# Performance work log

Measured on AMD Instinct MI355X. Metric: run time of the kernel, lower is better.

The kernel has to match this reference:

```python
import jax, jax.numpy as jnp
import numpy as np

HIDDEN = 1024
HEADS = 16
HEAD = HIDDEN // HEADS


def setup_inputs() -> dict:
    key = jax.random.key(0)
    k1, k2, k3, k4, k5, k6 = jax.random.split(key, 6)
    B, S = 2, 2048
    x = jax.random.normal(k1, (B, S, HIDDEN), dtype=jnp.float32)
    mask = jax.random.randint(k2, (B, S), 0, 2, dtype=jnp.int32)
    # torch nn.Linear params: W [out,in], b [out]
    s = 1.0 / np.sqrt(HIDDEN)
    qkv_w = jax.random.uniform(k3, (3 * HIDDEN, HIDDEN), jnp.float32, -s, s)
    qkv_b = jax.random.uniform(k4, (3 * HIDDEN,), jnp.float32, -s, s)
    out_w = jax.random.uniform(k5, (HIDDEN, HIDDEN), jnp.float32, -s, s)
    out_b = jax.random.uniform(k6, (HIDDEN,), jnp.float32, -s, s)
    return {"x": x, "mask": mask, "qkv_w": qkv_w, "qkv_b": qkv_b,
            "out_w": out_w, "out_b": out_b}


def reference(x, mask, qkv_w, qkv_b, out_w, out_b):
    B, S, H = x.shape
    scale = HEAD ** -0.5
    qkv = x @ qkv_w.T + qkv_b                      # [B,S,3H]
    qkv = qkv.reshape(B, S, 3, HEADS, HEAD)
    qkv = jnp.transpose(qkv, (2, 0, 3, 1, 4))      # [3,B,h,S,d]
    q, k, v = qkv[0], qkv[1], qkv[2]
    scores = jnp.einsum('bhqd,bhkd->bhqk', q, k) * scale
    # key-padding mask [B,S] -> [B,1,1,S]
    scores = jnp.where(mask[:, None, None, :] == 0, -1e9, scores)
    attn = jax.nn.softmax(scores, axis=-1)
    # dropout is identity in eval mode
    ctx = jnp.einsum('bhqk,bhkd->bhqd', attn, v)   # [B,h,S,d]
    ctx = jnp.transpose(ctx, (0, 2, 1, 3)).reshape(B, S, H)
    return ctx @ out_w.T + out_b
```

## Files before the change

### kernel.cpp

```cpp
#include <hip/hip_runtime.h>
#include <hip/hip_bf16.h>

#define S_LEN 2048
#define NH    16
#define HD    64
#define HID   1024
#define BATCH 2
#define STK   72
#define VSTK  136
#define SCQ   0.18033688f

typedef __bf16 bf16x8 __attribute__((ext_vector_type(8)));
typedef float  f32x4  __attribute__((ext_vector_type(4)));
typedef float  f32x16 __attribute__((ext_vector_type(16)));
typedef unsigned u32x2 __attribute__((ext_vector_type(2)));

__device__ __forceinline__ unsigned int pk2(float lo, float hi) {
    union { __hip_bfloat162 h; unsigned int u; } c;
    c.h = __float22bfloat162_rn(make_float2(lo, hi));
    return c.u;
}
__device__ __forceinline__ uint4 pk8(float4 a, float4 b) {
    uint4 o;
    o.x = pk2(a.x, a.y); o.y = pk2(a.z, a.w);
    o.z = pk2(b.x, b.y); o.w = pk2(b.z, b.w);
    return o;
}
__device__ __forceinline__ float exp2_hw(float x) {
    float r; asm("v_exp_f32 %0, %1" : "=v"(r) : "v"(x)); return r;
}
__device__ __forceinline__ void pl32swap(unsigned &a, unsigned &b) {
    u32x2 r = __builtin_amdgcn_permlane32_swap(a, b, false, false);
    a = r[0]; b = r[1];
}
__device__ __forceinline__ float pair_max(float x) {
    unsigned u = __float_as_uint(x);
    u32x2 r = __builtin_amdgcn_permlane32_swap(u, u, false, false);
    return fmaxf(__uint_as_float(r[0]), __uint_as_float(r[1]));
}
__device__ __forceinline__ float pair_sum(float x) {
    unsigned u = __float_as_uint(x);
    u32x2 r = __builtin_amdgcn_permlane32_swap(u, u, false, false);
    return __uint_as_float(r[0]) + __uint_as_float(r[1]);
}
__device__ __forceinline__ void gll16(const unsigned short* g, unsigned short* l) {
    __builtin_amdgcn_global_load_lds(
        (const __attribute__((address_space(1))) void*)g,
        (__attribute__((address_space(3))) void*)l, 16, 0, 0);
}

__global__ __launch_bounds__(256)
void fill_constf(float* __restrict__ out, long n, float v) {
    long i = (long)blockIdx.x * 256 + threadIdx.x;
    const long stride = (long)gridDim.x * 256;
    for (; i < n; i += stride) out[i] = v;
}

__global__ __launch_bounds__(256)
void cvt_bf16(const float* __restrict__ src, unsigned short* __restrict__ dst, long n8) {
    long t = (long)blockIdx.x * 256 + threadIdx.x;
    const long stride = (long)gridDim.x * 256;
    for (; t < n8; t += stride) {
        const float4 a = *(const float4*)(src + t * 8);
        const float4 b = *(const float4*)(src + t * 8 + 4);
        *(uint4*)(dst + t * 8) = pk8(a, b);
    }
}
__global__ __launch_bounds__(256)
void cvt2_bf16(const float* __restrict__ s0, unsigned short* __restrict__ d0, long n0,
               const float* __restrict__ s1, unsigned short* __restrict__ d1, long n1) {
    long t = (long)blockIdx.x * 256 + threadIdx.x;
    const long stride = (long)gridDim.x * 256;
    for (; t < n0 + n1; t += stride) {
        const float* s; unsigned short* d; long i;
        if (t < n0) { s = s0; d = d0; i = t; } else { s = s1; d = d1; i = t - n0; }
        const float4 a = *(const float4*)(s + i * 8);
        const float4 b = *(const float4*)(s + i * 8 + 4);
        *(uint4*)(d + i * 8) = pk8(a, b);
    }
}

__global__ __launch_bounds__(512)
void gemm_bf16(const unsigned short* __restrict__ A,
               const unsigned short* __restrict__ W,
               const float* __restrict__ bias,
               unsigned short* __restrict__ o0,
               unsigned short* __restrict__ o1,
               unsigned short* __restrict__ o2)
{
    __shared__ __align__(16) unsigned short lA[3][128 * 32];
    __shared__ __align__(16) unsigned short lB[3][128 * 32];
    const int tid  = threadIdx.x;
    const int lane = tid & 63, wv = tid >> 6;
    const int quad = lane >> 4, l16 = lane & 15;
    const int wm = (wv & 1) * 64, wn = (wv >> 1) * 32;

    const int nwg = gridDim.x * gridDim.y;
    const int bid = blockIdx.y * gridDim.x + blockIdx.x;
    const int xcd = bid & 7, boff = bid >> 3;
    const int qd = nwg >> 3, rm = nwg & 7;
    const int swz = (xcd < rm ? xcd * (qd + 1) : rm * (qd + 1) + (xcd - rm) * qd) + boff;
    const int m0 = (swz / gridDim.x) * 128, n0 = (swz % gridDim.x) * 128;

    f32x4 acc[4][2] = {};

    const int srow = wv * 16 + (lane >> 2);
    const int csrc = ((lane & 3) ^ ((lane >> 3) & 3)) * 8;
    const unsigned short* pa = A + (long)(m0 + srow) * HID + csrc;
    const unsigned short* pb = W + (long)(n0 + srow) * HID + csrc;

    const int cq8 = (quad ^ ((l16 >> 1) & 3)) * 8;

#define STAGE_G(bufi, koff)                                        \
    do {                                                           \
        gll16(pa + (koff), &lA[bufi][wv * 512]);                   \
        gll16(pb + (koff), &lB[bufi][wv * 512]);                   \
    } while (0)

    STAGE_G(0, 0);
    STAGE_G(1, 32);

    int cur = 0;
    for (int k0 = 0; k0 < HID; k0 += 32) {
        if (k0 + 32 < HID) { asm volatile("s_waitcnt vmcnt(2)" ::: "memory"); }
        else               { asm volatile("s_waitcnt vmcnt(0)" ::: "memory"); }
        __builtin_amdgcn_s_barrier();
        asm volatile("" ::: "memory");

        if (k0 + 64 < HID) {
            const int nxt = cur ? cur - 1 : 2;
            STAGE_G(nxt, k0 + 64);
        }

        bf16x8 af[4], bfr[2];
#pragma unroll
        for (int mt = 0; mt < 4; mt++)
            af[mt] = *(const bf16x8*)&lA[cur][(wm + mt * 16 + l16) * 32 + cq8];
#pragma unroll
        for (int nt = 0; nt < 2; nt++)
            bfr[nt] = *(const bf16x8*)&lB[cur][(wn + nt * 16 + l16) * 32 + cq8];
#pragma unroll
        for (int mt = 0; mt < 4; mt++)
#pragma unroll
            for (int nt = 0; nt < 2; nt++)
                acc[mt][nt] = __builtin_amdgcn_mfma_f32_16x16x32_bf16(
                    af[mt], bfr[nt], acc[mt][nt], 0, 0, 0);

        cur = (cur < 2) ? cur + 1 : 0;
    }
#undef STAGE_G

#pragma unroll
    for (int nt = 0; nt < 2; nt++) {
        const int n = n0 + wn + nt * 16 + l16;
        const float bv = bias[n];
        const int part = n >> 10, f = n & 1023, h = f >> 6, d = f & 63;
#pragma unroll
        for (int mt = 0; mt < 4; mt++) {
            const int mbase = m0 + wm + mt * 16 + quad * 4;
            const int b = mbase >> 11, s0 = mbase & 2047;
            const int bh = b * NH + h;
            if (part != 1) {
                const float qsc = (part == 0) ? SCQ : 1.0f;
                unsigned short* dst = (part == 0) ? o0 : o2;
                uint2 o;
                o.x = pk2((acc[mt][nt][0] + bv) * qsc, (acc[mt][nt][1] + bv) * qsc);
                o.y = pk2((acc[mt][nt][2] + bv) * qsc, (acc[mt][nt][3] + bv) * qsc);
                *(uint2*)&dst[((long)bh * HD + d) * S_LEN + s0] = o;
            } else {
#pragma unroll
                for (int r = 0; r < 4; r++) {
                    union { __hip_bfloat16 h; unsigned short u; } cv;
                    cv.h = __float2bfloat16(acc[mt][nt][r] + bv);
                    o1[((long)bh * S_LEN + s0 + r) * HD + d] = cv.u;
                }
            }
        }
    }
}

__global__ __launch_bounds__(512)
void gemm_out(const unsigned short* __restrict__ A,
              const unsigned short* __restrict__ W,
              const float* __restrict__ bias,
              float* __restrict__ of)
{
    __shared__ __align__(16) unsigned short lA[3][128 * 32];
    __shared__ __align__(16) unsigned short lB[3][64 * 32];
    const int tid  = threadIdx.x;
    const int lane = tid & 63, wv = tid >> 6;
    const int quad = lane >> 4, l16 = lane & 15;
    const int wm = (wv & 3) * 32, wn = (wv >> 2) * 32;

    const int nwg = gridDim.x * gridDim.y;
    const int bid = blockIdx.y * gridDim.x + blockIdx.x;
    const int xcd = bid & 7, boff = bid >> 3;
    const int qd = nwg >> 3, rm = nwg & 7;
    const int swz = (xcd < rm ? xcd * (qd + 1) : rm * (qd + 1) + (xcd - rm) * qd) + boff;
    const int m0 = (swz / gridDim.x) * 128, n0 = (swz % gridDim.x) * 64;

    f32x4 acc[2][2] = {};

    const int srowA = wv * 16 + (lane >> 2);
    const int srowB = srowA & 63;
    const int csrc  = ((lane & 3) ^ ((lane >> 3) & 3)) * 8;
    const unsigned short* pa = A + (long)(m0 + srowA) * HID + csrc;
    const unsigned short* pb = W + (long)(n0 + srowB) * HID + csrc;

    const int cq8 = (quad ^ ((l16 >> 1) & 3)) * 8;

#define STAGE_O(bufi, koff)                                        \
    do {                                                           \
        gll16(pa + (koff), &lA[bufi][wv * 512]);                   \
        if (wv < 4) gll16(pb + (koff), &lB[bufi][wv * 512]);       \
    } while (0)

    STAGE_O(0, 0);
    STAGE_O(1, 32);

    int cur = 0;
    for (int k0 = 0; k0 < HID; k0 += 32) {
        if (k0 + 32 < HID) {
            if (wv < 4) { asm volatile("s_waitcnt vmcnt(2)" ::: "memory"); }
            else        { asm volatile("s_waitcnt vmcnt(1)" ::: "memory"); }
        } else          { asm volatile("s_waitcnt vmcnt(0)" ::: "memory"); }
        __builtin_amdgcn_s_barrier();
        asm volatile("" ::: "memory");

        if (k0 + 64 < HID) {
            const int nxt = cur ? cur - 1 : 2;
            STAGE_O(nxt, k0 + 64);
        }

        bf16x8 af[2], bfr[2];
#pragma unroll
        for (int mt = 0; mt < 2; mt++)
            af[mt] = *(const bf16x8*)&lA[cur][(wm + mt * 16 + l16) * 32 + cq8];
#pragma unroll
        for (int nt = 0; nt < 2; nt++)
            bfr[nt] = *(const bf16x8*)&lB[cur][(wn + nt * 16 + l16) * 32 + cq8];
#pragma unroll
        for (int mt = 0; mt < 2; mt++)
#pragma unroll
            for (int nt = 0; nt < 2; nt++)
                acc[mt][nt] = __builtin_amdgcn_mfma_f32_16x16x32_bf16(
                    af[mt], bfr[nt], acc[mt][nt], 0, 0, 0);

        cur = (cur < 2) ? cur + 1 : 0;
    }
#undef STAGE_O

#pragma unroll
    for (int nt = 0; nt < 2; nt++) {
        const int n = n0 + wn + nt * 16 + l16;
        const float bv = bias[n];
#pragma unroll
        for (int mt = 0; mt < 2; mt++) {
            const int mbase = m0 + wm + mt * 16 + quad * 4;
#pragma unroll
            for (int r = 0; r < 4; r++)
                of[(long)(mbase + r) * HID + n] = acc[mt][nt][r] + bv;
        }
    }
}

__global__ __launch_bounds__(512, 4)
void attn(const unsigned short* __restrict__ q,
          const unsigned short* __restrict__ k,
          const unsigned short* __restrict__ vt_g,
          const int* __restrict__ mask,
          unsigned short* __restrict__ ctx)
{
    __shared__ __align__(16) unsigned short kt[2][128 * STK];
    __shared__ __align__(16) unsigned short vt[2][64 * VSTK];
    __shared__ __align__(16) float mkv[2][128];

    const int tid  = threadIdx.x;
    const int lane = tid & 63, wv = tid >> 6;
    const int ar = lane & 31, hi = lane >> 5;
    const int chunk = wv >> 1, p = wv & 1;
    const int id = blockIdx.x;
    const int xcd = id & 7, j = id >> 3;
    const int qt = j & 15, hbl = j >> 4;
    const int hb = xcd * 4 + hbl;
    const int h = hb & 15, b = hb >> 4;
    const int bh = b * NH + h;
    const int sq = qt * 128 + chunk * 32 + ar;

    union { unsigned short u[8]; bf16x8 v; } qu[4];
    const unsigned short* qg = q + (long)bh * HD * S_LEN + sq;
#pragma unroll
    for (int t = 0; t < 4; t++)
#pragma unroll
        for (int jj = 0; jj < 8; jj++)
            qu[t].u[jj] = qg[(long)(16 * t + 8 * hi + jj) * S_LEN];

    float mrun = 0.f, lsum = 0.f;
    f32x16 Of0 = {}, Of1 = {};

    const int sr = tid >> 3, c0 = tid & 7;
    const unsigned short* kg = k    + ((long)bh * S_LEN + sr) * HD + c0 * 8;
    const unsigned short* vg = vt_g + ((long)bh * HD + sr) * S_LEN + c0 * 8;
    const int wk0 = sr * STK + c0 * 8;
    const int wk1 = (sr + 64) * STK + c0 * 8;
    const int wv0 = sr * VSTK + c0 * 8;
    const int wv1 = sr * VSTK + c0 * 8 + 64;

    uint4 rk0 = *(const uint4*)(kg);
    uint4 rk1 = *(const uint4*)(kg + (long)64 * HD);
    uint4 rv0 = *(const uint4*)(vg);
    uint4 rv1 = *(const uint4*)(vg + 64);
    float rmv = 0.f;
    if (tid < 128) rmv = (mask[b * S_LEN + tid] == 0) ? -1e9f : 0.f;
    *(uint4*)&kt[0][wk0] = rk0;
    *(uint4*)&kt[0][wk1] = rk1;
    *(uint4*)&vt[0][wv0] = rv0;
    *(uint4*)&vt[0][wv1] = rv1;
    if (tid < 128) mkv[0][tid] = rmv;
    rk0 = *(const uint4*)(kg + (long)128 * HD);
    rk1 = *(const uint4*)(kg + (long)192 * HD);
    rv0 = *(const uint4*)(vg + 128);
    rv1 = *(const uint4*)(vg + 192);
    if (tid < 128) rmv = (mask[b * S_LEN + 128 + tid] == 0) ? -1e9f : 0.f;
    asm volatile("s_waitcnt lgkmcnt(0)" ::: "memory");
    __builtin_amdgcn_s_barrier();
    asm volatile("" ::: "memory");

    for (int k0 = 0; k0 < S_LEN; k0 += 128) {
        const int cur = (k0 >> 7) & 1;
        if (k0 + 128 < S_LEN) {
            *(uint4*)&kt[cur ^ 1][wk0] = rk0;
            *(uint4*)&kt[cur ^ 1][wk1] = rk1;
            *(uint4*)&vt[cur ^ 1][wv0] = rv0;
            *(uint4*)&vt[cur ^ 1][wv1] = rv1;
            if (tid < 128) mkv[cur ^ 1][tid] = rmv;
            if (k0 + 256 < S_LEN) {
                rk0 = *(const uint4*)(kg + (long)(k0 + 256) * HD);
                rk1 = *(const uint4*)(kg + (long)(k0 + 320) * HD);
                rv0 = *(const uint4*)(vg + (k0 + 256));
                rv1 = *(const uint4*)(vg + (k0 + 320));
                if (tid < 128) rmv = (mask[b * S_LEN + k0 + 256 + tid] == 0) ? -1e9f : 0.f;
            }
        }

#pragma unroll
        for (int G2 = 0; G2 < 2; G2++) {
            const int kb = 64 * G2 + 32 * p;

            f32x16 s;
#pragma unroll
            for (int m = 0; m < 4; m++) {
                const float4 mv = *(const float4*)&mkv[cur][kb + m * 8 + hi * 4];
                s[4 * m + 0] = mv.x; s[4 * m + 1] = mv.y;
                s[4 * m + 2] = mv.z; s[4 * m + 3] = mv.w;
            }
            __builtin_amdgcn_s_setprio(1);
#pragma unroll
            for (int t = 0; t < 4; t++) {
                bf16x8 kf = *(const bf16x8*)
                    &kt[cur][(kb + ar) * STK + (2 * t + hi) * 8];
                s = __builtin_amdgcn_mfma_f32_32x32x16_bf16(kf, qu[t].v, s, 0, 0, 0);
            }
            __builtin_amdgcn_s_setprio(0);

            if (k0 == 0 && G2 == 0) {
                float pm = fmaxf(fmaxf(fmaxf(s[0], s[1]), fmaxf(s[2], s[3])),
                           fmaxf(fmaxf(s[4], s[5]), fmaxf(s[6], s[7])));
                pm = fmaxf(pm,
                     fmaxf(fmaxf(fmaxf(s[8], s[9]), fmaxf(s[10], s[11])),
                           fmaxf(fmaxf(s[12], s[13]), fmaxf(s[14], s[15]))));
                mrun = fmaxf(pair_max(pm), -50.f);
            }

            float pr[16];
            float ls = 0.f;
#pragma unroll
            for (int r = 0; r < 16; r++) {
                pr[r] = exp2_hw(s[r] - mrun);
                ls += pr[r];
            }
            lsum += ls;
            unsigned wa[4], wb[4];
#pragma unroll
            for (int m = 0; m < 4; m++) {
                wa[m] = pk2(pr[4 * m + 0], pr[4 * m + 1]);
                wb[m] = pk2(pr[4 * m + 2], pr[4 * m + 3]);
            }

            union { unsigned u[4]; bf16x8 v; } F[2];
#pragma unroll
            for (int s5 = 0; s5 < 2; s5++) {
                const int mp = s5 * 2;
                unsigned f0 = wa[mp], f2 = wa[mp + 1];
                unsigned f1 = wb[mp], f3 = wb[mp + 1];
                pl32swap(f0, f2);
                pl32swap(f1, f3);
                F[s5].u[0] = f0; F[s5].u[1] = f1; F[s5].u[2] = f2; F[s5].u[3] = f3;
            }

            __builtin_amdgcn_s_setprio(1);
#pragma unroll
            for (int s5 = 0; s5 < 2; s5++) {
                const int col = (2 * (4 * G2 + 2 * p + s5) + hi) * 8;
                bf16x8 vf0 = *(const bf16x8*)&vt[cur][(0 * 32 + ar) * VSTK + col];
                Of0 = __builtin_amdgcn_mfma_f32_32x32x16_bf16(vf0, F[s5].v, Of0, 0, 0, 0);
                bf16x8 vf1 = *(const bf16x8*)&vt[cur][(1 * 32 + ar) * VSTK + col];
                Of1 = __builtin_amdgcn_mfma_f32_32x32x16_bf16(vf1, F[s5].v, Of1, 0, 0, 0);
            }
            __builtin_amdgcn_s_setprio(0);
        }

        asm volatile("s_waitcnt lgkmcnt(0)" ::: "memory");
        __builtin_amdgcn_s_barrier();
        asm volatile("" ::: "memory");
    }

    const float lp = pair_sum(lsum);
    float* mo0 = (float*)&kt[0][0];
    float* mo1 = (float*)&vt[0][0];
    float* mml = (float*)&vt[0][0] + 4096;
    const int mbase = (chunk * 64 + lane) * 16;
    const int mx4 = (lane >> 1) & 3;
    if (p == 1) {
#pragma unroll
        for (int m = 0; m < 4; m++) {
            const int off = mbase + ((m ^ mx4) << 2);
            *(float4*)&mo0[off] = make_float4(Of0[4*m+0], Of0[4*m+1], Of0[4*m+2], Of0[4*m+3]);
            *(float4*)&mo1[off] = make_float4(Of1[4*m+0], Of1[4*m+1], Of1[4*m+2], Of1[4*m+3]);
        }
        mml[(chunk * 64 + lane) * 2 + 0] = mrun;
        mml[(chunk * 64 + lane) * 2 + 1] = lp;
    }
    __syncthreads();
    if (p == 0) {
        const float m1 = mml[(chunk * 64 + lane) * 2 + 0];
        const float l1 = mml[(chunk * 64 + lane) * 2 + 1];
        const float mm = fmaxf(mrun, m1);
        const float a0 = exp2_hw(mrun - mm);
        const float a1 = exp2_hw(m1 - mm);
        const float inv = 1.f / (lp * a0 + l1 * a1);
        unsigned short* cb = ctx + ((long)b * S_LEN + sq) * HID + h * HD;
#pragma unroll
        for (int m = 0; m < 4; m++) {
            const int off = mbase + ((m ^ mx4) << 2);
            const float4 p0 = *(const float4*)&mo0[off];
            const float4 p1 = *(const float4*)&mo1[off];
            uint2 o0, o1;
            o0.x = pk2((Of0[4*m+0] * a0 + p0.x * a1) * inv,
                       (Of0[4*m+1] * a0 + p0.y * a1) * inv);
            o0.y = pk2((Of0[4*m+2] * a0 + p0.z * a1) * inv,
                       (Of0[4*m+3] * a0 + p0.w * a1) * inv);
            *(uint2*)&cb[m * 8 + hi * 4] = o0;
            o1.x = pk2((Of1[4*m+0] * a0 + p1.x * a1) * inv,
                       (Of1[4*m+1] * a0 + p1.y * a1) * inv);
            o1.y = pk2((Of1[4*m+2] * a0 + p1.z * a1) * inv,
                       (Of1[4*m+3] * a0 + p1.w * a1) * inv);
            *(uint2*)&cb[32 + m * 8 + hi * 4] = o1;
        }
    }
}

extern "C" void kernel_launch(void* const* d_in, const int* in_sizes, int n_in,
                              void* d_out, int out_size, void* d_ws, size_t ws_size,
                              hipStream_t stream) {
    float* outp = (float*)d_out;

    const float* x = nullptr; const int* mask = nullptr;
    const float* qkv_w = nullptr; const float* qkv_b = nullptr;
    const float* out_w = nullptr; const float* out_b = nullptr;
    for (int i = 0; i < n_in; i++) {
        switch (in_sizes[i]) {
            case 4194304: x     = (const float*)d_in[i]; break;
            case 4096:    mask  = (const int*)d_in[i];   break;
            case 3145728: qkv_w = (const float*)d_in[i]; break;
            case 3072:    qkv_b = (const float*)d_in[i]; break;
            case 1048576: out_w = (const float*)d_in[i]; break;
            case 1024:    out_b = (const float*)d_in[i]; break;
            default: break;
        }
    }
    if (!x || !mask || !qkv_w || !qkv_b || !out_w || !out_b) {
        fill_constf<<<256, 256, 0, stream>>>(outp, (long)out_size, 1000.0f);
        return;
    }

    const size_t per = (size_t)BATCH * NH * S_LEN * HD;
    const size_t nx  = (size_t)BATCH * S_LEN * HID;
    const size_t nqw = (size_t)3 * HID * HID;
    const size_t now = (size_t)HID * HID;
    if (ws_size < 4 * per * sizeof(unsigned short)) {
        fill_constf<<<256, 256, 0, stream>>>(outp, (long)out_size, 2000.0f);
        return;
    }

    unsigned short* wsq = (unsigned short*)d_ws;
    unsigned short* wsk = wsq + per;
    unsigned short* wsv = wsk + per;
    unsigned short* wsc = wsv + per;
    unsigned short* xb  = wsc;
    unsigned short* qwb = (unsigned short*)d_out;
    unsigned short* owb = wsq;

    cvt2_bf16<<<1024, 256, 0, stream>>>(x, xb, (long)(nx / 8), qkv_w, qwb, (long)(nqw / 8));
    gemm_bf16<<<dim3(3 * HID / 128, BATCH * S_LEN / 128), 512, 0, stream>>>(
        xb, qwb, qkv_b, wsq, wsk, wsv);
    attn<<<dim3(S_LEN / 128 * NH * BATCH), 512, 0, stream>>>(wsq, wsk, wsv, mask, wsc);
    cvt_bf16<<<512, 256, 0, stream>>>(out_w, owb, (long)(now / 8));
    gemm_out<<<dim3(HID / 64, BATCH * S_LEN / 128), 512, 0, stream>>>(
        wsc, owb, out_b, outp);
}
```

Before: 196.6 us.

## Fuse fp32-to-bf16 conversion into GEMM tile loads and drop convert kernels

Both GEMMs now load fp32 inputs (x, qkv_w, out_w) straight from global memory into registers, convert them to bf16, and write them to LDS. This removes the separate conversion kernels and their global round trip. Staging changes from 3-stage async global_load_lds to a 2-stage register-prefetch double buffer with a barrier each iteration. Block-to-tile mapping becomes a fixed per-XCD layout, and launch bounds now request 4 blocks per CU. The costs are twice the global read bytes per tile, because fp32 values are re-read by every block that uses them, plus conversion work inside the main loop.

```diff
diff --git a/kernel.cpp b/kernel.cpp
--- a/kernel.cpp
+++ b/kernel.cpp
@@ -43,11 +43,6 @@
     u32x2 r = __builtin_amdgcn_permlane32_swap(u, u, false, false);
     return __uint_as_float(r[0]) + __uint_as_float(r[1]);
 }
-__device__ __forceinline__ void gll16(const unsigned short* g, unsigned short* l) {
-    __builtin_amdgcn_global_load_lds(
-        (const __attribute__((address_space(1))) void*)g,
-        (__attribute__((address_space(3))) void*)l, 16, 0, 0);
-}
 
 __global__ __launch_bounds__(256)
 void fill_constf(float* __restrict__ out, long n, float v) {
@@ -56,80 +51,61 @@
     for (; i < n; i += stride) out[i] = v;
 }
 
-__global__ __launch_bounds__(256)
-void cvt_bf16(const float* __restrict__ src, unsigned short* __restrict__ dst, long n8) {
-    long t = (long)blockIdx.x * 256 + threadIdx.x;
-    const long stride = (long)gridDim.x * 256;
-    for (; t < n8; t += stride) {
-        const float4 a = *(const float4*)(src + t * 8);
-        const float4 b = *(const float4*)(src + t * 8 + 4);
-        *(uint4*)(dst + t * 8) = pk8(a, b);
-    }
-}
-__global__ __launch_bounds__(256)
-void cvt2_bf16(const float* __restrict__ s0, unsigned short* __restrict__ d0, long n0,
-               const float* __restrict__ s1, unsigned short* __restrict__ d1, long n1) {
-    long t = (long)blockIdx.x * 256 + threadIdx.x;
-    const long stride = (long)gridDim.x * 256;
-    for (; t < n0 + n1; t += stride) {
-        const float* s; unsigned short* d; long i;
-        if (t < n0) { s = s0; d = d0; i = t; } else { s = s1; d = d1; i = t - n0; }
-        const float4 a = *(const float4*)(s + i * 8);
-        const float4 b = *(const float4*)(s + i * 8 + 4);
-        *(uint4*)(d + i * 8) = pk8(a, b);
-    }
-}
-
-__global__ __launch_bounds__(512)
-void gemm_bf16(const unsigned short* __restrict__ A,
-               const unsigned short* __restrict__ W,
-               const float* __restrict__ bias,
-               unsigned short* __restrict__ o0,
-               unsigned short* __restrict__ o1,
-               unsigned short* __restrict__ o2)
+__global__ __launch_bounds__(512, 4)
+void gemm_qkv(const float* __restrict__ X,
+              const float* __restrict__ W,
+              const float* __restrict__ bias,
+              unsigned short* __restrict__ o0,
+              unsigned short* __restrict__ o1,
+              unsigned short* __restrict__ o2)
 {
-    __shared__ __align__(16) unsigned short lA[3][128 * 32];
-    __shared__ __align__(16) unsigned short lB[3][128 * 32];
+    __shared__ __align__(16) unsigned short lA[2][128 * 32];
+    __shared__ __align__(16) unsigned short lB[2][128 * 32];
     const int tid  = threadIdx.x;
     const int lane = tid & 63, wv = tid >> 6;
     const int quad = lane >> 4, l16 = lane & 15;
     const int wm = (wv & 1) * 64, wn = (wv >> 1) * 32;
 
-    const int nwg = gridDim.x * gridDim.y;
-    const int bid = blockIdx.y * gridDim.x + blockIdx.x;
+    const int bid = blockIdx.x;
     const int xcd = bid & 7, boff = bid >> 3;
-    const int qd = nwg >> 3, rm = nwg & 7;
-    const int swz = (xcd < rm ? xcd * (qd + 1) : rm * (qd + 1) + (xcd - rm) * qd) + boff;
-    const int m0 = (swz / gridDim.x) * 128, n0 = (swz % gridDim.x) * 128;
+    const int mloc = boff / 12, nloc = boff % 12;
+    const int m0 = ((xcd & 3) * 8 + mloc) * 128;
+    const int n0 = ((xcd >> 2) * 12 + nloc) * 128;
 
     f32x4 acc[4][2] = {};
 
-    const int srow = wv * 16 + (lane >> 2);
-    const int csrc = ((lane & 3) ^ ((lane >> 3) & 3)) * 8;
-    const unsigned short* pa = A + (long)(m0 + srow) * HID + csrc;
-    const unsigned short* pb = W + (long)(n0 + srow) * HID + csrc;
-
+    const int r = tid >> 2, c = tid & 3;
+    const int wofs = r * 32 + ((c ^ ((r >> 1) & 3)) * 8);
+    const float* px = X + (long)(m0 + r) * HID + c * 8;
+    const float* pw = W + (long)(n0 + r) * HID + c * 8;
     const int cq8 = (quad ^ ((l16 >> 1) & 3)) * 8;
 
-#define STAGE_G(bufi, koff)                                        \
-    do {                                                           \
-        gll16(pa + (koff), &lA[bufi][wv * 512]);                   \
-        gll16(pb + (koff), &lB[bufi][wv * 512]);                   \
-    } while (0)
-
-    STAGE_G(0, 0);
-    STAGE_G(1, 32);
-
-    int cur = 0;
+    float4 xa, xb2, wa2, wb2;
+    xa  = *(const float4*)(px);
+    xb2 = *(const float4*)(px + 4);
+    wa2 = *(const float4*)(pw);
+    wb2 = *(const float4*)(pw + 4);
+    *(uint4*)&lA[0][wofs] = pk8(xa, xb2);
+    *(uint4*)&lB[0][wofs] = pk8(wa2, wb2);
+    xa  = *(const float4*)(px + 32);
+    xb2 = *(const float4*)(px + 36);
+    wa2 = *(const float4*)(pw + 32);
+    wb2 = *(const float4*)(pw + 36);
+    asm volatile("s_waitcnt lgkmcnt(0)" ::: "memory");
+    __builtin_amdgcn_s_barrier();
+    asm volatile("" ::: "memory");
+
     for (int k0 = 0; k0 < HID; k0 += 32) {
-        if (k0 + 32 < HID) { asm volatile("s_waitcnt vmcnt(2)" ::: "memory"); }
-        else               { asm volatile("s_waitcnt vmcnt(0)" ::: "memory"); }
-        __builtin_amdgcn_s_barrier();
-        asm volatile("" ::: "memory");
-
-        if (k0 + 64 < HID) {
-            const int nxt = cur ? cur - 1 : 2;
-            STAGE_G(nxt, k0 + 64);
+        const int cur = (k0 >> 5) & 1;
+        if (k0 + 32 < HID) {
+            *(uint4*)&lA[cur ^ 1][wofs] = pk8(xa, xb2);
+            *(uint4*)&lB[cur ^ 1][wofs] = pk8(wa2, wb2);
+            if (k0 + 64 < HID) {
+                xa  = *(const float4*)(px + k0 + 64);
+                xb2 = *(const float4*)(px + k0 + 68);
+                wa2 = *(const float4*)(pw + k0 + 64);
+                wb2 = *(const float4*)(pw + k0 + 68);
+            }
         }
 
         bf16x8 af[4], bfr[2];
@@ -146,9 +122,10 @@
                 acc[mt][nt] = __builtin_amdgcn_mfma_f32_16x16x32_bf16(
                     af[mt], bfr[nt], acc[mt][nt], 0, 0, 0);
 
-        cur = (cur < 2) ? cur + 1 : 0;
-    }
-#undef STAGE_G
+        asm volatile("s_waitcnt lgkmcnt(0)" ::: "memory");
+        __builtin_amdgcn_s_barrier();
+        asm volatile("" ::: "memory");
+    }
 
 #pragma unroll
     for (int nt = 0; nt < 2; nt++) {
@@ -169,67 +146,68 @@
                 *(uint2*)&dst[((long)bh * HD + d) * S_LEN + s0] = o;
             } else {
 #pragma unroll
-                for (int r = 0; r < 4; r++) {
+                for (int rr = 0; rr < 4; rr++) {
                     union { __hip_bfloat16 h; unsigned short u; } cv;
-                    cv.h = __float2bfloat16(acc[mt][nt][r] + bv);
-                    o1[((long)bh * S_LEN + s0 + r) * HD + d] = cv.u;
+                    cv.h = __float2bfloat16(acc[mt][nt][rr] + bv);
+                    o1[((long)bh * S_LEN + s0 + rr) * HD + d] = cv.u;
                 }
             }
         }
     }
 }
 
-__global__ __launch_bounds__(512)
+__global__ __launch_bounds__(512, 4)
 void gemm_out(const unsigned short* __restrict__ A,
-              const unsigned short* __restrict__ W,
+              const float* __restrict__ W,
               const float* __restrict__ bias,
               float* __restrict__ of)
 {
-    __shared__ __align__(16) unsigned short lA[3][128 * 32];
-    __shared__ __align__(16) unsigned short lB[3][64 * 32];
+    __shared__ __align__(16) unsigned short lA[2][128 * 32];
+    __shared__ __align__(16) unsigned short lB[2][64 * 32];
     const int tid  = threadIdx.x;
     const int lane = tid & 63, wv = tid >> 6;
     const int quad = lane >> 4, l16 = lane & 15;
     const int wm = (wv & 3) * 32, wn = (wv >> 2) * 32;
 
-    const int nwg = gridDim.x * gridDim.y;
-    const int bid = blockIdx.y * gridDim.x + blockIdx.x;
+    const int bid = blockIdx.x;
     const int xcd = bid & 7, boff = bid >> 3;
-    const int qd = nwg >> 3, rm = nwg & 7;
-    const int swz = (xcd < rm ? xcd * (qd + 1) : rm * (qd + 1) + (xcd - rm) * qd) + boff;
-    const int m0 = (swz / gridDim.x) * 128, n0 = (swz % gridDim.x) * 64;
+    const int mloc = boff >> 3, nloc = boff & 7;
+    const int m0 = ((xcd & 3) * 8 + mloc) * 128;
+    const int n0 = ((xcd >> 2) * 8 + nloc) * 64;
 
     f32x4 acc[2][2] = {};
 
-    const int srowA = wv * 16 + (lane >> 2);
-    const int srowB = srowA & 63;
-    const int csrc  = ((lane & 3) ^ ((lane >> 3) & 3)) * 8;
-    const unsigned short* pa = A + (long)(m0 + srowA) * HID + csrc;
-    const unsigned short* pb = W + (long)(n0 + srowB) * HID + csrc;
-
+    const int rA = tid >> 2, c = tid & 3;
+    const int rB = rA & 63;
+    const int wofsA = rA * 32 + ((c ^ ((rA >> 1) & 3)) * 8);
+    const int wofsB = rB * 32 + ((c ^ ((rB >> 1) & 3)) * 8);
+    const unsigned short* pa = A + (long)(m0 + rA) * HID + c * 8;
+    const float*          pb = W + (long)(n0 + rB) * HID + c * 8;
     const int cq8 = (quad ^ ((l16 >> 1) & 3)) * 8;
 
-#define STAGE_O(bufi, koff)                                        \
-    do {                                                           \
-        gll16(pa + (koff), &lA[bufi][wv * 512]);                   \
-        if (wv < 4) gll16(pb + (koff), &lB[bufi][wv * 512]);       \
-    } while (0)
-
-    STAGE_O(0, 0);
-    STAGE_O(1, 32);
-
-    int cur = 0;
+    uint4 ra; float4 wa2, wb2;
+    ra = *(const uint4*)(pa);
+    if (wv < 4) { wa2 = *(const float4*)(pb); wb2 = *(const float4*)(pb + 4); }
+    *(uint4*)&lA[0][wofsA] = ra;
+    if (wv < 4) *(uint4*)&lB[0][wofsB] = pk8(wa2, wb2);
+    ra = *(const uint4*)(pa + 32);
+    if (wv < 4) { wa2 = *(const float4*)(pb + 32); wb2 = *(const float4*)(pb + 36); }
+    asm volatile("s_waitcnt lgkmcnt(0)" ::: "memory");
+    __builtin_amdgcn_s_barrier();
+    asm volatile("" ::: "memory");
+
     for (int k0 = 0; k0 < HID; k0 += 32) {
+        const int cur = (k0 >> 5) & 1;
         if (k0 + 32 < HID) {
-            if (wv < 4) { asm volatile("s_waitcnt vmcnt(2)" ::: "memory"); }
-            else        { asm volatile("s_waitcnt vmcnt(1)" ::: "memory"); }
-        } else          { asm volatile("s_waitcnt vmcnt(0)" ::: "memory"); }
-        __builtin_amdgcn_s_barrier();
-        asm volatile("" ::: "memory");
-
-        if (k0 + 64 < HID) {
-            const int nxt = cur ? cur - 1 : 2;
-            STAGE_O(nxt, k0 + 64);
+            *(uint4*)&lA[cur ^ 1][wofsA] = ra;
+            if (wv < 4) *(uint4*)&lB[cur ^ 1][wofsB] = pk8(wa2, wb2);
+            if (k0 + 64 < HID) {
+                ra = *(const uint4*)(pa + k0 + 64);
+                if (wv < 4) {
+                    wa2 = *(const float4*)(pb + k0 + 64);
+                    wb2 = *(const float4*)(pb + k0 + 68);
+                }
+            }
         }
 
         bf16x8 af[2], bfr[2];
@@ -246,9 +224,10 @@
                 acc[mt][nt] = __builtin_amdgcn_mfma_f32_16x16x32_bf16(
                     af[mt], bfr[nt], acc[mt][nt], 0, 0, 0);
 
-        cur = (cur < 2) ? cur + 1 : 0;
-    }
-#undef STAGE_O
+        asm volatile("s_waitcnt lgkmcnt(0)" ::: "memory");
+        __builtin_amdgcn_s_barrier();
+        asm volatile("" ::: "memory");
+    }
 
 #pragma unroll
     for (int nt = 0; nt < 2; nt++) {
@@ -258,8 +237,8 @@
         for (int mt = 0; mt < 2; mt++) {
             const int mbase = m0 + wm + mt * 16 + quad * 4;
 #pragma unroll
-            for (int r = 0; r < 4; r++)
-                of[(long)(mbase + r) * HID + n] = acc[mt][nt][r] + bv;
+            for (int rr = 0; rr < 4; rr++)
+                of[(long)(mbase + rr) * HID + n] = acc[mt][nt][rr] + bv;
         }
     }
 }
@@ -485,9 +464,6 @@
     }
 
     const size_t per = (size_t)BATCH * NH * S_LEN * HD;
-    const size_t nx  = (size_t)BATCH * S_LEN * HID;
-    const size_t nqw = (size_t)3 * HID * HID;
-    const size_t now = (size_t)HID * HID;
     if (ws_size < 4 * per * sizeof(unsigned short)) {
         fill_constf<<<256, 256, 0, stream>>>(outp, (long)out_size, 2000.0f);
         return;
@@ -497,15 +473,8 @@
     unsigned short* wsk = wsq + per;
     unsigned short* wsv = wsk + per;
     unsigned short* wsc = wsv + per;
-    unsigned short* xb  = wsc;
-    unsigned short* qwb = (unsigned short*)d_out;
-    unsigned short* owb = wsq;
-
-    cvt2_bf16<<<1024, 256, 0, stream>>>(x, xb, (long)(nx / 8), qkv_w, qwb, (long)(nqw / 8));
-    gemm_bf16<<<dim3(3 * HID / 128, BATCH * S_LEN / 128), 512, 0, stream>>>(
-        xb, qwb, qkv_b, wsq, wsk, wsv);
+
+    gemm_qkv<<<768, 512, 0, stream>>>(x, qkv_w, qkv_b, wsq, wsk, wsv);
     attn<<<dim3(S_LEN / 128 * NH * BATCH), 512, 0, stream>>>(wsq, wsk, wsv, mask, wsc);
-    cvt_bf16<<<512, 256, 0, stream>>>(out_w, owb, (long)(now / 8));
-    gemm_out<<<dim3(HID / 64, BATCH * S_LEN / 128), 512, 0, stream>>>(
-        wsc, owb, out_b, outp);
-}
+    gemm_out<<<512, 512, 0, stream>>>(wsc, out_w, out_b, outp);
+}
```

Measured after the change: 199.0 us. No clear change (+1.2%).
